# Kernel optimization log

Hardware: AMD Instinct MI355X
Metric: run time of the kernel (lower is better)

## Reference

```python
import jax, jax.numpy as jnp
import numpy as np

NUM_EMBED = 1024
HEAD_SIZE = 64
B, T = 4, 4096

def setup_inputs() -> dict:
    key = jax.random.key(0)
    kx, kq, kk, kv = jax.random.split(key, 4)
    scale = NUM_EMBED ** -0.5
    return {
        "x": jax.random.normal(kx, (B, T, NUM_EMBED), dtype=jnp.float32),
        "Wq": jax.random.normal(kq, (NUM_EMBED, HEAD_SIZE), dtype=jnp.float32) * scale,
        "Wk": jax.random.normal(kk, (NUM_EMBED, HEAD_SIZE), dtype=jnp.float32) * scale,
        "Wv": jax.random.normal(kv, (NUM_EMBED, HEAD_SIZE), dtype=jnp.float32) * scale,
    }

def reference(x, Wq, Wk, Wv):
    # x: [B,T,C]; Wq/Wk/Wv: [C,H]
    q = jnp.einsum('btc,ch->bth', x, Wq)
    k = jnp.einsum('btc,ch->bth', x, Wk)
    v = jnp.einsum('btc,ch->bth', x, Wv)
    Tq = x.shape[1]
    att = jnp.einsum('bth,bsh->bts', q, k) * (k.shape[-1] ** -0.5)  # [B,T,T]
    causal = jnp.tril(jnp.ones((Tq, Tq), dtype=bool))
    att = jnp.where(causal, att, -jnp.inf)
    att = jax.nn.softmax(att, axis=-1)
    # dropout p=0 (eval mode): identity
    out = jnp.einsum('bts,bsh->bth', att, v)  # [B,T,H]
    return out
```

## Files before the change

kernel.cpp:

```cpp
#include <hip/hip_runtime.h>

#define B_ 4
#define T_ 4096
#define C_ 1024
#define H_ 64

typedef _Float16 half8  __attribute__((ext_vector_type(8)));
typedef _Float16 half4_ __attribute__((ext_vector_type(4)));
typedef float    floatx4 __attribute__((ext_vector_type(4)));

#define MFMA16(a, b, c) __builtin_amdgcn_mfma_f32_16x16x32_f16(a, b, c, 0, 0, 0)

__global__ __launch_bounds__(256) void pack_w_kn(
    const float* __restrict__ Wq, const float* __restrict__ Wk,
    const float* __restrict__ Wv, _Float16* __restrict__ Wt2)
{
    const int idx  = blockIdx.x * 256 + threadIdx.x;
    const int mt   = idx >> 14;
    const int j    = (idx >> 10) & 15;
    const int f    = (idx >> 9) & 1;
    const int lane = (idx >> 3) & 63;
    const int jj   = idx & 7;
    const int q = lane >> 4, c = lane & 15;
    const int k  = j * 64 + f * 32 + q * 8 + jj;
    const int hp = mt * 16 + c;
    const float* W = (hp < 64) ? Wq : (hp < 128) ? Wk : Wv;
    Wt2[idx] = (_Float16)W[k * H_ + (hp & 63)];
}

__global__ __launch_bounds__(512) void qkv_kn(
    const float* __restrict__ x, const _Float16* __restrict__ Wt2,
    _Float16* __restrict__ Qpk, _Float16* __restrict__ Kpk,
    _Float16* __restrict__ Vpk)
{
    __shared__ _Float16 xs[2][32][72];
    const int tid  = threadIdx.x;
    const int lane = tid & 63, w = tid >> 6;
    const int q    = lane >> 4, c = lane & 15;
    const int nt   = w & 1;
    const int mg   = w >> 1;
    const int row0 = blockIdx.x * 32;

    const int srow = tid >> 4, scol = (tid & 15) * 4;
    const float* xg = x + (size_t)(row0 + srow) * C_ + scol;

    floatx4 acc[3];
    #pragma unroll
    for (int i = 0; i < 3; ++i) acc[i] = floatx4{0.f, 0.f, 0.f, 0.f};

    float4 g = *(const float4*)xg;

    for (int j = 0; j < 16; ++j) {
        half4_ hv;
        hv[0] = (_Float16)g.x; hv[1] = (_Float16)g.y;
        hv[2] = (_Float16)g.z; hv[3] = (_Float16)g.w;
        *(half4_*)(&xs[j & 1][srow][scol]) = hv;
        __syncthreads();
        if (j < 15) g = *(const float4*)(xg + (j + 1) * 64);

        const _Float16* xrow = &xs[j & 1][nt * 16 + c][q * 8];
        const half8 b0 = *(const half8*)xrow;
        const half8 b1 = *(const half8*)(xrow + 32);

        half8 a[6];
        #pragma unroll
        for (int i = 0; i < 3; ++i) {
            const size_t fb = ((size_t)((mg * 3 + i) * 16 + j) * 2) * 512 + lane * 8;
            a[i * 2]     = *(const half8*)(Wt2 + fb);
            a[i * 2 + 1] = *(const half8*)(Wt2 + fb + 512);
        }
        #pragma unroll
        for (int i = 0; i < 3; ++i) {
            acc[i] = MFMA16(a[i * 2],     b0, acc[i]);
            acc[i] = MFMA16(a[i * 2 + 1], b1, acc[i]);
        }
    }

    const int row = row0 + nt * 16 + c;
    const int b = row >> 12, t4 = row & (T_ - 1);
    const int kt = t4 >> 6;
    const size_t tbase = ((size_t)b * 64 + kt) * 4096;
    const int mtk = (t4 >> 4) & 3;
    const int kk  = t4 & 63;

    #pragma unroll
    for (int i = 0; i < 3; ++i) {
        const int gi = mg * 3 + i;
        if (gi < 4) {
            half4_ v;
            #pragma unroll
            for (int r = 0; r < 4; ++r) v[r] = (_Float16)acc[i][r];
            const int qa = (gi * 2 + (q >> 1)) & 3;
            *(half4_*)(Qpk + ((size_t)b * 256 + (t4 >> 4)) * 1024
                       + ((size_t)((gi >> 1) * 64 + qa * 16 + c)) * 8
                       + (q & 1) * 4) = v;
        } else if (gi < 8) {
            half4_ v;
            #pragma unroll
            for (int r = 0; r < 4; ++r) v[r] = (_Float16)acc[i][r];
            const int e  = gi - 4;
            const int f  = e >> 1;
            const int qa = (e * 2 + (q >> 1)) & 3;
            *(half4_*)(Kpk + tbase + ((size_t)(mtk * 2 + f) * 64 + qa * 16 + c) * 8
                       + (q & 1) * 4) = v;
        } else {
            const int mtv = gi - 8;
            const int qa = (kk >> 3) & 3, fv = kk >> 5, jv = kk & 7;
            #pragma unroll
            for (int r = 0; r < 4; ++r) {
                const int cv = q * 4 + r;
                Vpk[tbase + ((size_t)(mtv * 2 + fv) * 64 + qa * 16 + cv) * 8 + jv]
                    = (_Float16)acc[i][r];
            }
        }
    }
}

__global__ __launch_bounds__(512, 4) void attn_kn(
    const _Float16* __restrict__ Qpk, const _Float16* __restrict__ Kpk,
    const _Float16* __restrict__ Vpk, float* __restrict__ out)
{
    __shared__ __align__(16) char smem[36864];
    const int lane = threadIdx.x & 63;
    const int w    = threadIdx.x >> 6;
    const int q    = lane >> 4, c = lane & 15;
    const int b    = blockIdx.y;
    const int t    = (blockIdx.y & 1) ? (int)blockIdx.x
                                      : 255 - (int)blockIdx.x;
    const int row0 = t * 16;
    const int grow = b * T_ + row0;
    const int nk   = (t >> 2) + 1;

    _Float16* Pw = (_Float16*)smem + w * 2304;

    const _Float16* qp = Qpk + ((size_t)b * 256 + t) * 1024 + (size_t)lane * 8;
    half8 bq0 = *(const half8*)qp;
    half8 bq1 = *(const half8*)(qp + 512);
    const _Float16 qs = (_Float16)0.18033688f;
    bq0 *= qs; bq1 *= qs;

    floatx4 o[4];
    #pragma unroll
    for (int i = 0; i < 4; ++i) o[i] = floatx4{0.f, 0.f, 0.f, 0.f};
    float m = -3.0e38f, l = 0.f;

    for (int kt = w; kt < nk; kt += 8) {
        const int kb = kt * 64;
        const _Float16* Kt = Kpk + ((size_t)b * 64 + kt) * 4096;
        const _Float16* Vt = Vpk + ((size_t)b * 64 + kt) * 4096;
        half8 a0[4], a1[4];

        #pragma unroll
        for (int mt = 0; mt < 4; ++mt) {
            a0[mt] = *(const half8*)(Kt + ((size_t)(mt * 2)     * 64 + lane) * 8);
            a1[mt] = *(const half8*)(Kt + ((size_t)(mt * 2 + 1) * 64 + lane) * 8);
        }
        floatx4 s[4];
        #pragma unroll
        for (int mt = 0; mt < 4; ++mt) {
            floatx4 z = floatx4{0.f, 0.f, 0.f, 0.f};
            z = MFMA16(a0[mt], bq0, z);
            s[mt] = MFMA16(a1[mt], bq1, z);
        }
        #pragma unroll
        for (int mt = 0; mt < 4; ++mt) {
            a0[mt] = *(const half8*)(Vt + ((size_t)(mt * 2)     * 64 + lane) * 8);
            a1[mt] = *(const half8*)(Vt + ((size_t)(mt * 2 + 1) * 64 + lane) * 8);
        }

        if (kt == nk - 1) {
            #pragma unroll
            for (int mt = 0; mt < 4; ++mt)
                #pragma unroll
                for (int r = 0; r < 4; ++r)
                    if (kb + mt * 16 + q * 4 + r > row0 + c) s[mt][r] = -3.0e38f;
        }

        float mx = s[0][0];
        #pragma unroll
        for (int mt = 0; mt < 4; ++mt)
            #pragma unroll
            for (int r = 0; r < 4; ++r) mx = fmaxf(mx, s[mt][r]);
        mx = fmaxf(mx, __shfl_xor(mx, 16, 64));
        mx = fmaxf(mx, __shfl_xor(mx, 32, 64));
        const float mn    = fmaxf(m, mx);
        const float alpha = exp2f(m - mn);
        float p[4][4];
        float sl = 0.f;
        #pragma unroll
        for (int mt = 0; mt < 4; ++mt)
            #pragma unroll
            for (int r = 0; r < 4; ++r) {
                p[mt][r] = exp2f(s[mt][r] - mn);
                sl += p[mt][r];
            }
        sl += __shfl_xor(sl, 16, 64);
        sl += __shfl_xor(sl, 32, 64);
        l = l * alpha + sl;
        m = mn;
        #pragma unroll
        for (int mt = 0; mt < 4; ++mt)
            #pragma unroll
            for (int r = 0; r < 4; ++r) o[mt][r] *= alpha;

        _Float16* pl = Pw + ((kt >> 3) & 1) * 1152 + c * 72;
        #pragma unroll
        for (int mt = 0; mt < 4; ++mt) {
            half4_ ph;
            #pragma unroll
            for (int r = 0; r < 4; ++r) ph[r] = (_Float16)p[mt][r];
            *(half4_*)(pl + mt * 16 + q * 4) = ph;
        }
        const half8 bp0 = *(const half8*)(pl + q * 8);
        const half8 bp1 = *(const half8*)(pl + 32 + q * 8);

        #pragma unroll
        for (int mt = 0; mt < 4; ++mt) {
            o[mt] = MFMA16(a0[mt], bp0, o[mt]);
            o[mt] = MFMA16(a1[mt], bp1, o[mt]);
        }
    }

    __syncthreads();
    float* Ol = (float*)smem;
    float* Ml = (float*)(smem + 34816);
    float* Ll = (float*)(smem + 35328);
    if (q == 0) Ml[w * 16 + c] = m;
    __syncthreads();
    float M = Ml[c];
    #pragma unroll
    for (int w2 = 1; w2 < 8; ++w2) M = fmaxf(M, Ml[w2 * 16 + c]);
    const float alpha = exp2f(m - M);
    if (q == 0) Ll[w * 16 + c] = l * alpha;
    #pragma unroll
    for (int mt = 0; mt < 4; ++mt)
        #pragma unroll
        for (int r = 0; r < 4; ++r)
            Ol[w * 1088 + (mt * 16 + q * 4 + r) * 17 + c] = o[mt][r] * alpha;
    __syncthreads();

    float L = 0.f;
    #pragma unroll
    for (int w2 = 0; w2 < 8; ++w2) L += Ll[w2 * 16 + c];
    const float inv = 1.f / L;
    const int h0 = w * 8 + q * 2;
    float ox = 0.f, oy = 0.f;
    #pragma unroll
    for (int w2 = 0; w2 < 8; ++w2) {
        ox += Ol[w2 * 1088 + h0 * 17 + c];
        oy += Ol[w2 * 1088 + (h0 + 1) * 17 + c];
    }
    float2 st; st.x = ox * inv; st.y = oy * inv;
    *(float2*)(out + (size_t)(grow + c) * H_ + h0) = st;
}

extern "C" void kernel_launch(void* const* d_in, const int* in_sizes, int n_in,
                              void* d_out, int out_size, void* d_ws, size_t ws_size,
                              hipStream_t stream) {
    const float* x  = (const float*)d_in[0];
    const float* Wq = (const float*)d_in[1];
    const float* Wk = (const float*)d_in[2];
    const float* Wv = (const float*)d_in[3];
    float* out = (float*)d_out;

    _Float16* ws = (_Float16*)d_ws;
    _Float16* Wt2 = ws;
    _Float16* Qpk = ws + 196608;
    _Float16* Kpk = Qpk + 1048576;
    _Float16* Vpk = Kpk + 1048576;

    hipLaunchKernelGGL(pack_w_kn, dim3(768), dim3(256), 0, stream, Wq, Wk, Wv, Wt2);
    hipLaunchKernelGGL(qkv_kn, dim3((B_ * T_) / 32), dim3(512), 0, stream,
                       x, Wt2, Qpk, Kpk, Vpk);
    hipLaunchKernelGGL(attn_kn, dim3(T_ / 16, B_), dim3(512), 0, stream,
                       Qpk, Kpk, Vpk, out);
}
```

Measured before the change: 146.2 us.

## Pair causal query tiles per block, prefetch K, and stage x via direct-to-LDS loads

The attention kernel now launches half as many blocks. Each block handles two query tiles, t and 255-t, so every block gets the same causal work. The K loop also prefetches the next K tile into registers while the current one is processed. The projection kernel now uses global_load_lds to copy fp32 x straight into an XOR-swizzled shared buffer and converts it to fp16 on read, dropping the register round-trip. In exchange it uses twice the LDS for x, puts the two tiles in series with extra barriers, and adds register pressure from the prefetched K.

Result: slower. 152.7 us (+4.5%).

```diff
diff --git a/kernel.cpp b/kernel.cpp
--- a/kernel.cpp
+++ b/kernel.cpp
@@ -10,6 +10,12 @@
 typedef float    floatx4 __attribute__((ext_vector_type(4)));
 
 #define MFMA16(a, b, c) __builtin_amdgcn_mfma_f32_16x16x32_f16(a, b, c, 0, 0, 0)
+
+__device__ __forceinline__ void glds16(const float* g, float* l) {
+    __builtin_amdgcn_global_load_lds(
+        (const __attribute__((address_space(1))) unsigned int*)g,
+        (__attribute__((address_space(3))) unsigned int*)l, 16, 0, 0);
+}
 
 __global__ __launch_bounds__(256) void pack_w_kn(
     const float* __restrict__ Wq, const float* __restrict__ Wk,
@@ -33,7 +39,7 @@
     _Float16* __restrict__ Qpk, _Float16* __restrict__ Kpk,
     _Float16* __restrict__ Vpk)
 {
-    __shared__ _Float16 xs[2][32][72];
+    __shared__ float xs[2][32][64];
     const int tid  = threadIdx.x;
     const int lane = tid & 63, w = tid >> 6;
     const int q    = lane >> 4, c = lane & 15;
@@ -41,26 +47,37 @@
     const int mg   = w >> 1;
     const int row0 = blockIdx.x * 32;
 
-    const int srow = tid >> 4, scol = (tid & 15) * 4;
-    const float* xg = x + (size_t)(row0 + srow) * C_ + scol;
+    const int grow = tid >> 4;
+    const int pch  = tid & 15;
+    const int lch  = pch ^ (grow & 7);
+    const float* xsrc = x + (size_t)(row0 + grow) * C_ + lch * 4;
 
     floatx4 acc[3];
     #pragma unroll
     for (int i = 0; i < 3; ++i) acc[i] = floatx4{0.f, 0.f, 0.f, 0.f};
 
-    float4 g = *(const float4*)xg;
+    glds16(xsrc, &xs[0][w * 4][0]);
 
     for (int j = 0; j < 16; ++j) {
-        half4_ hv;
-        hv[0] = (_Float16)g.x; hv[1] = (_Float16)g.y;
-        hv[2] = (_Float16)g.z; hv[3] = (_Float16)g.w;
-        *(half4_*)(&xs[j & 1][srow][scol]) = hv;
-        __syncthreads();
-        if (j < 15) g = *(const float4*)(xg + (j + 1) * 64);
-
-        const _Float16* xrow = &xs[j & 1][nt * 16 + c][q * 8];
-        const half8 b0 = *(const half8*)xrow;
-        const half8 b1 = *(const half8*)(xrow + 32);
+        __syncthreads();
+        if (j < 15)
+            glds16(xsrc + (j + 1) * 64, &xs[(j + 1) & 1][w * 4][0]);
+
+        const float* rowp = &xs[j & 1][nt * 16 + c][0];
+        const int e = c & 7;
+        const float4 f0 = *(const float4*)(rowp + ((2 * q)     ^ e) * 4);
+        const float4 f1 = *(const float4*)(rowp + ((2 * q + 1) ^ e) * 4);
+        const float4 f2 = *(const float4*)(rowp + ((8 + 2 * q) ^ e) * 4);
+        const float4 f3 = *(const float4*)(rowp + ((9 + 2 * q) ^ e) * 4);
+        half8 b0, b1;
+        b0[0] = (_Float16)f0.x; b0[1] = (_Float16)f0.y;
+        b0[2] = (_Float16)f0.z; b0[3] = (_Float16)f0.w;
+        b0[4] = (_Float16)f1.x; b0[5] = (_Float16)f1.y;
+        b0[6] = (_Float16)f1.z; b0[7] = (_Float16)f1.w;
+        b1[0] = (_Float16)f2.x; b1[1] = (_Float16)f2.y;
+        b1[2] = (_Float16)f2.z; b1[3] = (_Float16)f2.w;
+        b1[4] = (_Float16)f3.x; b1[5] = (_Float16)f3.y;
+        b1[6] = (_Float16)f3.z; b1[7] = (_Float16)f3.w;
 
         half8 a[6];
         #pragma unroll
@@ -98,9 +115,9 @@
             half4_ v;
             #pragma unroll
             for (int r = 0; r < 4; ++r) v[r] = (_Float16)acc[i][r];
-            const int e  = gi - 4;
-            const int f  = e >> 1;
-            const int qa = (e * 2 + (q >> 1)) & 3;
+            const int e2 = gi - 4;
+            const int f  = e2 >> 1;
+            const int qa = (e2 * 2 + (q >> 1)) & 3;
             *(half4_*)(Kpk + tbase + ((size_t)(mtk * 2 + f) * 64 + qa * 16 + c) * 8
                        + (q & 1) * 4) = v;
         } else {
@@ -125,133 +142,151 @@
     const int w    = threadIdx.x >> 6;
     const int q    = lane >> 4, c = lane & 15;
     const int b    = blockIdx.y;
-    const int t    = (blockIdx.y & 1) ? (int)blockIdx.x
-                                      : 255 - (int)blockIdx.x;
-    const int row0 = t * 16;
-    const int grow = b * T_ + row0;
-    const int nk   = (t >> 2) + 1;
 
     _Float16* Pw = (_Float16*)smem + w * 2304;
-
-    const _Float16* qp = Qpk + ((size_t)b * 256 + t) * 1024 + (size_t)lane * 8;
-    half8 bq0 = *(const half8*)qp;
-    half8 bq1 = *(const half8*)(qp + 512);
-    const _Float16 qs = (_Float16)0.18033688f;
-    bq0 *= qs; bq1 *= qs;
-
-    floatx4 o[4];
-    #pragma unroll
-    for (int i = 0; i < 4; ++i) o[i] = floatx4{0.f, 0.f, 0.f, 0.f};
-    float m = -3.0e38f, l = 0.f;
-
-    for (int kt = w; kt < nk; kt += 8) {
-        const int kb = kt * 64;
-        const _Float16* Kt = Kpk + ((size_t)b * 64 + kt) * 4096;
-        const _Float16* Vt = Vpk + ((size_t)b * 64 + kt) * 4096;
-        half8 a0[4], a1[4];
-
-        #pragma unroll
-        for (int mt = 0; mt < 4; ++mt) {
-            a0[mt] = *(const half8*)(Kt + ((size_t)(mt * 2)     * 64 + lane) * 8);
-            a1[mt] = *(const half8*)(Kt + ((size_t)(mt * 2 + 1) * 64 + lane) * 8);
-        }
-        floatx4 s[4];
-        #pragma unroll
-        for (int mt = 0; mt < 4; ++mt) {
-            floatx4 z = floatx4{0.f, 0.f, 0.f, 0.f};
-            z = MFMA16(a0[mt], bq0, z);
-            s[mt] = MFMA16(a1[mt], bq1, z);
-        }
-        #pragma unroll
-        for (int mt = 0; mt < 4; ++mt) {
-            a0[mt] = *(const half8*)(Vt + ((size_t)(mt * 2)     * 64 + lane) * 8);
-            a1[mt] = *(const half8*)(Vt + ((size_t)(mt * 2 + 1) * 64 + lane) * 8);
-        }
-
-        if (kt == nk - 1) {
-            #pragma unroll
-            for (int mt = 0; mt < 4; ++mt)
-                #pragma unroll
-                for (int r = 0; r < 4; ++r)
-                    if (kb + mt * 16 + q * 4 + r > row0 + c) s[mt][r] = -3.0e38f;
-        }
-
-        float mx = s[0][0];
-        #pragma unroll
-        for (int mt = 0; mt < 4; ++mt)
-            #pragma unroll
-            for (int r = 0; r < 4; ++r) mx = fmaxf(mx, s[mt][r]);
-        mx = fmaxf(mx, __shfl_xor(mx, 16, 64));
-        mx = fmaxf(mx, __shfl_xor(mx, 32, 64));
-        const float mn    = fmaxf(m, mx);
-        const float alpha = exp2f(m - mn);
-        float p[4][4];
-        float sl = 0.f;
-        #pragma unroll
-        for (int mt = 0; mt < 4; ++mt)
-            #pragma unroll
-            for (int r = 0; r < 4; ++r) {
-                p[mt][r] = exp2f(s[mt][r] - mn);
-                sl += p[mt][r];
-            }
-        sl += __shfl_xor(sl, 16, 64);
-        sl += __shfl_xor(sl, 32, 64);
-        l = l * alpha + sl;
-        m = mn;
-        #pragma unroll
-        for (int mt = 0; mt < 4; ++mt)
-            #pragma unroll
-            for (int r = 0; r < 4; ++r) o[mt][r] *= alpha;
-
-        _Float16* pl = Pw + ((kt >> 3) & 1) * 1152 + c * 72;
-        #pragma unroll
-        for (int mt = 0; mt < 4; ++mt) {
-            half4_ ph;
-            #pragma unroll
-            for (int r = 0; r < 4; ++r) ph[r] = (_Float16)p[mt][r];
-            *(half4_*)(pl + mt * 16 + q * 4) = ph;
-        }
-        const half8 bp0 = *(const half8*)(pl + q * 8);
-        const half8 bp1 = *(const half8*)(pl + 32 + q * 8);
-
-        #pragma unroll
-        for (int mt = 0; mt < 4; ++mt) {
-            o[mt] = MFMA16(a0[mt], bp0, o[mt]);
-            o[mt] = MFMA16(a1[mt], bp1, o[mt]);
-        }
-    }
-
-    __syncthreads();
     float* Ol = (float*)smem;
     float* Ml = (float*)(smem + 34816);
     float* Ll = (float*)(smem + 35328);
-    if (q == 0) Ml[w * 16 + c] = m;
-    __syncthreads();
-    float M = Ml[c];
-    #pragma unroll
-    for (int w2 = 1; w2 < 8; ++w2) M = fmaxf(M, Ml[w2 * 16 + c]);
-    const float alpha = exp2f(m - M);
-    if (q == 0) Ll[w * 16 + c] = l * alpha;
-    #pragma unroll
-    for (int mt = 0; mt < 4; ++mt)
-        #pragma unroll
-        for (int r = 0; r < 4; ++r)
-            Ol[w * 1088 + (mt * 16 + q * 4 + r) * 17 + c] = o[mt][r] * alpha;
-    __syncthreads();
-
-    float L = 0.f;
-    #pragma unroll
-    for (int w2 = 0; w2 < 8; ++w2) L += Ll[w2 * 16 + c];
-    const float inv = 1.f / L;
-    const int h0 = w * 8 + q * 2;
-    float ox = 0.f, oy = 0.f;
-    #pragma unroll
-    for (int w2 = 0; w2 < 8; ++w2) {
-        ox += Ol[w2 * 1088 + h0 * 17 + c];
-        oy += Ol[w2 * 1088 + (h0 + 1) * 17 + c];
+
+    #pragma unroll 1
+    for (int hf = 0; hf < 2; ++hf) {
+        const int t    = hf ? (int)blockIdx.x : 255 - (int)blockIdx.x;
+        const int row0 = t * 16;
+        const int grow = b * T_ + row0;
+        const int nk   = (t >> 2) + 1;
+
+        const _Float16* qp = Qpk + ((size_t)b * 256 + t) * 1024 + (size_t)lane * 8;
+        half8 bq0 = *(const half8*)qp;
+        half8 bq1 = *(const half8*)(qp + 512);
+        const _Float16 qs = (_Float16)0.18033688f;
+        bq0 *= qs; bq1 *= qs;
+
+        floatx4 o[4];
+        #pragma unroll
+        for (int i = 0; i < 4; ++i) o[i] = floatx4{0.f, 0.f, 0.f, 0.f};
+        float m = -3.0e38f, l = 0.f;
+
+        half8 ka[4], kb8[4];
+        if (w < nk) {
+            const _Float16* Kt = Kpk + ((size_t)b * 64 + w) * 4096;
+            #pragma unroll
+            for (int mt = 0; mt < 4; ++mt) {
+                ka[mt]  = *(const half8*)(Kt + ((size_t)(mt * 2)     * 64 + lane) * 8);
+                kb8[mt] = *(const half8*)(Kt + ((size_t)(mt * 2 + 1) * 64 + lane) * 8);
+            }
+        }
+
+        for (int kt = w; kt < nk; kt += 8) {
+            const int kb = kt * 64;
+
+            floatx4 s[4];
+            #pragma unroll
+            for (int mt = 0; mt < 4; ++mt) {
+                floatx4 z = floatx4{0.f, 0.f, 0.f, 0.f};
+                z = MFMA16(ka[mt], bq0, z);
+                s[mt] = MFMA16(kb8[mt], bq1, z);
+            }
+
+            const _Float16* Vt = Vpk + ((size_t)b * 64 + kt) * 4096;
+            half8 va[4], vb[4];
+            #pragma unroll
+            for (int mt = 0; mt < 4; ++mt) {
+                va[mt] = *(const half8*)(Vt + ((size_t)(mt * 2)     * 64 + lane) * 8);
+                vb[mt] = *(const half8*)(Vt + ((size_t)(mt * 2 + 1) * 64 + lane) * 8);
+            }
+            {
+                const int ktn = (kt + 8 < nk) ? kt + 8 : kt;
+                const _Float16* Kt = Kpk + ((size_t)b * 64 + ktn) * 4096;
+                #pragma unroll
+                for (int mt = 0; mt < 4; ++mt) {
+                    ka[mt]  = *(const half8*)(Kt + ((size_t)(mt * 2)     * 64 + lane) * 8);
+                    kb8[mt] = *(const half8*)(Kt + ((size_t)(mt * 2 + 1) * 64 + lane) * 8);
+                }
+            }
+
+            if (kt == nk - 1) {
+                #pragma unroll
+                for (int mt = 0; mt < 4; ++mt)
+                    #pragma unroll
+                    for (int r = 0; r < 4; ++r)
+                        if (kb + mt * 16 + q * 4 + r > row0 + c)
+                            s[mt][r] = -3.0e38f;
+            }
+
+            float mx = s[0][0];
+            #pragma unroll
+            for (int mt = 0; mt < 4; ++mt)
+                #pragma unroll
+                for (int r = 0; r < 4; ++r) mx = fmaxf(mx, s[mt][r]);
+            mx = fmaxf(mx, __shfl_xor(mx, 16, 64));
+            mx = fmaxf(mx, __shfl_xor(mx, 32, 64));
+            const float mn    = fmaxf(m, mx);
+            const float alpha = exp2f(m - mn);
+            float sl = 0.f;
+            #pragma unroll
+            for (int mt = 0; mt < 4; ++mt)
+                #pragma unroll
+                for (int r = 0; r < 4; ++r) {
+                    s[mt][r] = exp2f(s[mt][r] - mn);
+                    sl += s[mt][r];
+                }
+            sl += __shfl_xor(sl, 16, 64);
+            sl += __shfl_xor(sl, 32, 64);
+            l = l * alpha + sl;
+            m = mn;
+            #pragma unroll
+            for (int mt = 0; mt < 4; ++mt)
+                #pragma unroll
+                for (int r = 0; r < 4; ++r) o[mt][r] *= alpha;
+
+            _Float16* pl = Pw + ((kt >> 3) & 1) * 1152 + c * 72;
+            #pragma unroll
+            for (int mt = 0; mt < 4; ++mt) {
+                half4_ ph;
+                #pragma unroll
+                for (int r = 0; r < 4; ++r) ph[r] = (_Float16)s[mt][r];
+                *(half4_*)(pl + mt * 16 + q * 4) = ph;
+            }
+            const half8 bp0 = *(const half8*)(pl + q * 8);
+            const half8 bp1 = *(const half8*)(pl + 32 + q * 8);
+
+            #pragma unroll
+            for (int mt = 0; mt < 4; ++mt) {
+                o[mt] = MFMA16(va[mt], bp0, o[mt]);
+                o[mt] = MFMA16(vb[mt], bp1, o[mt]);
+            }
+        }
+
+        __syncthreads();
+        if (q == 0) Ml[w * 16 + c] = m;
+        __syncthreads();
+        float M = Ml[c];
+        #pragma unroll
+        for (int w2 = 1; w2 < 8; ++w2) M = fmaxf(M, Ml[w2 * 16 + c]);
+        const float alpha = exp2f(m - M);
+        if (q == 0) Ll[w * 16 + c] = l * alpha;
+        #pragma unroll
+        for (int mt = 0; mt < 4; ++mt)
+            #pragma unroll
+            for (int r = 0; r < 4; ++r)
+                Ol[w * 1088 + (mt * 16 + q * 4 + r) * 17 + c] = o[mt][r] * alpha;
+        __syncthreads();
+
+        float L = 0.f;
+        #pragma unroll
+        for (int w2 = 0; w2 < 8; ++w2) L += Ll[w2 * 16 + c];
+        const float inv = 1.f / L;
+        const int h0 = w * 8 + q * 2;
+        float ox = 0.f, oy = 0.f;
+        #pragma unroll
+        for (int w2 = 0; w2 < 8; ++w2) {
+            ox += Ol[w2 * 1088 + h0 * 17 + c];
+            oy += Ol[w2 * 1088 + (h0 + 1) * 17 + c];
+        }
+        float2 st; st.x = ox * inv; st.y = oy * inv;
+        *(float2*)(out + (size_t)(grow + c) * H_ + h0) = st;
+        __syncthreads();
     }
-    float2 st; st.x = ox * inv; st.y = oy * inv;
-    *(float2*)(out + (size_t)(grow + c) * H_ + h0) = st;
 }
 
 extern "C" void kernel_launch(void* const* d_in, const int* in_sizes, int n_in,
@@ -272,6 +307,6 @@
     hipLaunchKernelGGL(pack_w_kn, dim3(768), dim3(256), 0, stream, Wq, Wk, Wv, Wt2);
     hipLaunchKernelGGL(qkv_kn, dim3((B_ * T_) / 32), dim3(512), 0, stream,
                        x, Wt2, Qpk, Kpk, Vpk);
-    hipLaunchKernelGGL(attn_kn, dim3(T_ / 16, B_), dim3(512), 0, stream,
+    hipLaunchKernelGGL(attn_kn, dim3(T_ / 32, B_), dim3(512), 0, stream,
                        Qpk, Kpk, Vpk, out);
 }
```
